# Optimization experiments

Measured on AMD Instinct MI355X. Metric: run time of the kernel, lower is better.

Reference implementation:

```python
import jax, jax.numpy as jnp
import numpy as np


def setup_inputs() -> dict:
    key = jax.random.key(0)
    k1, k2, k3, k4 = jax.random.split(key, 4)
    B, C, T, H, W = 2, 64, 8, 48, 48
    C2 = C // 2
    x_in = jax.random.normal(k1, (B, C, T, H, W), dtype=jnp.float32)
    # per-time-slice 1x1 conv weights (theta/phi pairs), kaiming-ish scale
    theta_w = jax.random.normal(k2, (T, C2, C), dtype=jnp.float32) / np.sqrt(C)
    phi_w = jax.random.normal(k3, (T, C2, C), dtype=jnp.float32) / np.sqrt(C)
    out_w = jax.random.normal(k4, (C, C), dtype=jnp.float32) / np.sqrt(C)
    return {"x_in": x_in, "theta_w": theta_w, "phi_w": phi_w, "out_w": out_w}


def reference(x_in, theta_w, phi_w, out_w):
    B, C, T, H, W = x_in.shape
    C2 = theta_w.shape[1]
    P = H * W
    # [B, T, C, P] layout: flatten spatial, move time next to batch
    x = jnp.transpose(x_in, (0, 2, 1, 3, 4)).reshape(B, T, C, P)
    # per-slice 1x1 convs == per-slice channel matmuls with slice-specific weights
    theta = jnp.einsum("toc,btcp->btop", theta_w, x)  # [B,T,C2,P]
    phi = jnp.einsum("toc,btcp->btop", phi_w, x)      # [B,T,C2,P]
    scale = 1.0 / jnp.sqrt(jnp.asarray(C2, dtype=x_in.dtype))
    scores = jnp.einsum("btcp,btcq->btpq", theta, phi) * scale  # [B,T,P,P]
    attn = jax.nn.softmax(scores, axis=-1)
    f = jnp.einsum("btpq,btcq->btcp", attn, x)  # value = raw x, [B,T,C,P]
    # conv_out: 1x1x1 Conv3d (pointwise over channels), then residual
    out = jnp.einsum("oc,btcp->btop", out_w, f)
    out = jnp.transpose(out.reshape(B, T, C, H, W), (0, 2, 1, 3, 4))
    return out + x_in
```

## Files before the change

### kernel.cpp

```cpp
#include <hip/hip_runtime.h>
#include <hip/hip_bf16.h>

#define CC 64
#define TT 8
#define PP 2304
#define C2 32
#define BT 16
#define NKT 36
#define QKT 9
#define SCALE2 0.25503486f

using h8 = __attribute__((ext_vector_type(8))) _Float16;
using h4 = __attribute__((ext_vector_type(4))) _Float16;
using f4 = __attribute__((ext_vector_type(4))) float;

#if __has_builtin(__builtin_amdgcn_exp2f)
#define EXP2(v) __builtin_amdgcn_exp2f(v)
#else
#define EXP2(v) exp2f(v)
#endif

#define SWIZ_BT(xcd, g) ((xcd) + 8 * ((g) & 1))


__global__ __launch_bounds__(512) void k_prep(
    const float* __restrict__ x, const float* __restrict__ tw,
    const float* __restrict__ pw, _Float16* __restrict__ thf,
    _Float16* __restrict__ rec) {
  const int qt = blockIdx.y >> 1, bt = SWIZ_BT(blockIdx.x, blockIdx.y);
  const int b = bt >> 3, t = bt & 7;
  const int tid = threadIdx.x;
  const int wv = tid >> 6, lane = tid & 63;
  const int quad = lane >> 4, l15 = lane & 15;

  __shared__ __align__(16) float x_s[64][68];
  __shared__ __align__(16) _Float16 th_s[4][16][32];
  __shared__ __align__(16) _Float16 ph_s[4][16][32];

  const size_t xslice = ((size_t)b * CC * TT + t) * PP;
  const int qg0 = qt * 64;
  _Float16* rb = rec + (size_t)(bt * NKT + qt) * 6144;
  const f4 zero = {0.f, 0.f, 0.f, 0.f};

  {
    const int l16 = tid & 15;
    const int crow = tid >> 4;
#pragma unroll
    for (int ppass = 0; ppass < 2; ppass++) {
      const int c = ppass * 32 + crow;
      float4 u = *reinterpret_cast<const float4*>(
          &x[xslice + (size_t)c * (TT * PP) + qg0 + l16 * 4]);
      x_s[l16 * 4 + 0][c] = u.x;
      x_s[l16 * 4 + 1][c] = u.y;
      x_s[l16 * 4 + 2][c] = u.z;
      x_s[l16 * 4 + 3][c] = u.w;
    }
  }
  __syncthreads();

  if (wv < 4) {
    h8 bx[2];
#pragma unroll
    for (int ks = 0; ks < 2; ks++) {
      const float* row = &x_s[wv * 16 + l15][ks * 32 + quad * 8];
      float4 u0 = *reinterpret_cast<const float4*>(row);
      float4 u1 = *reinterpret_cast<const float4*>(row + 4);
      bx[ks][0] = (_Float16)u0.x; bx[ks][1] = (_Float16)u0.y;
      bx[ks][2] = (_Float16)u0.z; bx[ks][3] = (_Float16)u0.w;
      bx[ks][4] = (_Float16)u1.x; bx[ks][5] = (_Float16)u1.y;
      bx[ks][6] = (_Float16)u1.z; bx[ks][7] = (_Float16)u1.w;
    }

    const float* twt = tw + t * C2 * CC;
    const float* pwt = pw + t * C2 * CC;
    f4 accT[2] = {zero, zero}, accP[2] = {zero, zero};
#pragma unroll
    for (int mt = 0; mt < 2; mt++)
#pragma unroll
      for (int ks = 0; ks < 2; ks++) {
        const float* wr = twt + (mt * 16 + l15) * CC + ks * 32 + quad * 8;
        const float* pr = pwt + (mt * 16 + l15) * CC + ks * 32 + quad * 8;
        float4 a0 = *reinterpret_cast<const float4*>(wr);
        float4 a1 = *reinterpret_cast<const float4*>(wr + 4);
        float4 p0 = *reinterpret_cast<const float4*>(pr);
        float4 p1 = *reinterpret_cast<const float4*>(pr + 4);
        h8 at = {(_Float16)a0.x, (_Float16)a0.y, (_Float16)a0.z,
                 (_Float16)a0.w, (_Float16)a1.x, (_Float16)a1.y,
                 (_Float16)a1.z, (_Float16)a1.w};
        h8 ap = {(_Float16)p0.x, (_Float16)p0.y, (_Float16)p0.z,
                 (_Float16)p0.w, (_Float16)p1.x, (_Float16)p1.y,
                 (_Float16)p1.z, (_Float16)p1.w};
        accT[mt] = __builtin_amdgcn_mfma_f32_16x16x32_f16(at, bx[ks],
                                                          accT[mt], 0, 0, 0);
        accP[mt] = __builtin_amdgcn_mfma_f32_16x16x32_f16(ap, bx[ks],
                                                          accP[mt], 0, 0, 0);
      }

#pragma unroll
    for (int mt = 0; mt < 2; mt++) {
      h4 tv, pv;
#pragma unroll
      for (int r = 0; r < 4; r++) {
        tv[r] = (_Float16)(accT[mt][r] * SCALE2);
        pv[r] = (_Float16)accP[mt][r];
      }
      *reinterpret_cast<h4*>(&th_s[wv][l15][mt * 16 + quad * 4]) = tv;
      *reinterpret_cast<h4*>(&ph_s[wv][l15][mt * 16 + quad * 4]) = pv;
    }

    h8 tfrag = *reinterpret_cast<const h8*>(&th_s[wv][l15][quad * 8]);
    *reinterpret_cast<h8*>(
        thf + (((size_t)(bt * NKT + qt) * 4 + wv) * 64 + lane) * 8) = tfrag;

    h8 pfrag = *reinterpret_cast<const h8*>(&ph_s[wv][l15][quad * 8]);
    *reinterpret_cast<h8*>(rb + wv * 512 + lane * 8) = pfrag;
  } else {
    const int w2 = wv - 4;
    const int g = w2 >> 1;
#pragma unroll
    for (int ct2 = 0; ct2 < 2; ct2++) {
      const int ct = (w2 & 1) * 2 + ct2;
      h8 v;
#pragma unroll
      for (int j = 0; j < 4; j++) {
        v[j] = (_Float16)x_s[32 * g + quad * 4 + j][ct * 16 + l15];
        v[4 + j] = (_Float16)x_s[32 * g + 16 + quad * 4 + j][ct * 16 + l15];
      }
      *reinterpret_cast<h8*>(rb + 2048 + (g * 4 + ct) * 512 + lane * 8) = v;
    }
  }
}

__global__ __launch_bounds__(256, 3) void k_attn(
    const float* __restrict__ x, const _Float16* __restrict__ thf,
    const _Float16* __restrict__ rec, const float* __restrict__ ow,
    float* __restrict__ out) {
  const int strip = blockIdx.y >> 1;
  const int bt = SWIZ_BT(blockIdx.x, blockIdx.y);
  const int b = bt >> 3, t = bt & 7;
  const int tid = threadIdx.x;
  const int kg = tid >> 6, lane = tid & 63;
  const int quad = lane >> 4, l15 = lane & 15;

  __shared__ __align__(16) float exch[4 * 3 * 16 * 64];
  __shared__ float exl[4 * 3 * 64];

  h8 bth[3];
#pragma unroll
  for (int pf = 0; pf < 3; pf++)
    bth[pf] = *reinterpret_cast<const h8*>(
        thf + (((size_t)bt * 144 + strip * 3 + pf) * 64 + lane) * 8);

  const _Float16* recb =
      rec + ((size_t)bt * NKT + (size_t)kg * QKT) * 6144 + lane * 8;

  const f4 zero = {0.f, 0.f, 0.f, 0.f};
  f4 O[4][3];
#pragma unroll
  for (int ct = 0; ct < 4; ct++)
#pragma unroll
    for (int pf = 0; pf < 3; pf++) O[ct][pf] = zero;
  float lsum[3] = {0.f, 0.f, 0.f};

  h8 buf[12];

#pragma unroll
  for (int i = 0; i < QKT; i++) {
    const _Float16* _p = recb + (size_t)i * 6144;
#pragma unroll
    for (int j = 0; j < 12; j++)
      buf[j] = *reinterpret_cast<const h8*>(_p + j * 512);

#pragma unroll
    for (int pf = 0; pf < 3; pf++) {
      f4 s[4];
#pragma unroll
      for (int nt = 0; nt < 4; nt++)
        s[nt] = __builtin_amdgcn_mfma_f32_16x16x32_f16(buf[nt], bth[pf], zero,
                                                       0, 0, 0);
#pragma unroll
      for (int g = 0; g < 2; g++) {
        h8 bw;
#pragma unroll
        for (int r = 0; r < 4; r++) {
          float w0 = EXP2(s[2 * g][r]);
          float w1 = EXP2(s[2 * g + 1][r]);
          lsum[pf] += w0 + w1;
          bw[r] = (_Float16)w0;
          bw[4 + r] = (_Float16)w1;
        }
#pragma unroll
        for (int ct = 0; ct < 4; ct++)
          O[ct][pf] = __builtin_amdgcn_mfma_f32_16x16x32_f16(
              buf[4 + g * 4 + ct], bw, O[ct][pf], 0, 0, 0);
      }
    }
  }

#pragma unroll
  for (int pf = 0; pf < 3; pf++) {
    lsum[pf] += __shfl_xor(lsum[pf], 16);
    lsum[pf] += __shfl_xor(lsum[pf], 32);
  }

#pragma unroll
  for (int pf = 0; pf < 3; pf++) {
#pragma unroll
    for (int ct = 0; ct < 4; ct++)
#pragma unroll
      for (int r = 0; r < 4; r++)
        exch[((kg * 3 + pf) * 16 + ct * 4 + r) * 64 + lane] = O[ct][pf][r];
    exl[(kg * 3 + pf) * 64 + lane] = lsum[pf];
  }
  __syncthreads();

  if (kg < 3) {
    float ls = 0.f;
#pragma unroll
    for (int src = 0; src < 4; src++) ls += exl[(src * 3 + kg) * 64 + lane];
    const float inv = 1.f / ls;

    h4 bf[4];
#pragma unroll
    for (int ct = 0; ct < 4; ct++)
#pragma unroll
      for (int r = 0; r < 4; r++) {
        float acc = 0.f;
#pragma unroll
        for (int src = 0; src < 4; src++)
          acc += exch[((src * 3 + kg) * 16 + ct * 4 + r) * 64 + lane];
        bf[ct][r] = (_Float16)(acc * inv);
      }

    f4 D3[4] = {zero, zero, zero, zero};
#pragma unroll
    for (int mt = 0; mt < 4; mt++)
#pragma unroll
      for (int ct = 0; ct < 4; ct++) {
        const float* wrow =
            ow + (size_t)(mt * 16 + l15) * CC + ct * 16 + quad * 4;
        float4 u = *reinterpret_cast<const float4*>(wrow);
        h4 aw = {(_Float16)u.x, (_Float16)u.y, (_Float16)u.z, (_Float16)u.w};
        D3[mt] =
            __builtin_amdgcn_mfma_f32_16x16x16f16(aw, bf[ct], D3[mt], 0, 0, 0);
      }

    const int p0 = strip * 48 + kg * 16 + l15;
#pragma unroll
    for (int mt = 0; mt < 4; mt++)
#pragma unroll
      for (int r = 0; r < 4; r++) {
        const int o = mt * 16 + quad * 4 + r;
        const size_t base = ((size_t)(b * CC + o) * TT + t) * PP + p0;
        out[base] = D3[mt][r] + x[base];
      }
  }
}

extern "C" void kernel_launch(void* const* d_in, const int* in_sizes, int n_in,
                              void* d_out, int out_size, void* d_ws,
                              size_t ws_size, hipStream_t stream) {
  (void)in_sizes; (void)n_in; (void)out_size; (void)ws_size;
  const float* x = (const float*)d_in[0];
  const float* tw = (const float*)d_in[1];
  const float* pw = (const float*)d_in[2];
  const float* ow = (const float*)d_in[3];
  float* out = (float*)d_out;

  _Float16* thf = (_Float16*)d_ws;
  _Float16* rec = thf + (size_t)BT * NKT * 4 * 64 * 8;

  k_prep<<<dim3(8, 72), 512, 0, stream>>>(x, tw, pw, thf, rec);
  k_attn<<<dim3(8, 96), 256, 0, stream>>>(x, thf, rec, ow, out);
}
```

Before: 96.37 us.

## Split attention work by query tile per wave instead of key range

Each of three waves now owns one 16-query tile and iterates over all 36 key tiles, replacing the previous scheme where four waves split the key range and combined partial outputs through shared memory. This removes the LDS exchange, the barrier and the idle fourth wave in the epilogue, and cuts accumulator register use. In exchange, each wave loads every K/V tile independently, which triples global/L2 reads of the rec buffer per block, and each block has fewer waves to hide latency.

```diff
diff --git a/kernel.cpp b/kernel.cpp
--- a/kernel.cpp
+++ b/kernel.cpp
@@ -7,7 +7,6 @@
 #define C2 32
 #define BT 16
 #define NKT 36
-#define QKT 9
 #define SCALE2 0.25503486f
 
 using h8 = __attribute__((ext_vector_type(8))) _Float16;
@@ -131,7 +130,7 @@
   }
 }
 
-__global__ __launch_bounds__(256, 3) void k_attn(
+__global__ __launch_bounds__(192, 3) void k_attn(
     const float* __restrict__ x, const _Float16* __restrict__ thf,
     const _Float16* __restrict__ rec, const float* __restrict__ ow,
     float* __restrict__ out) {
@@ -139,122 +138,81 @@
   const int bt = SWIZ_BT(blockIdx.x, blockIdx.y);
   const int b = bt >> 3, t = bt & 7;
   const int tid = threadIdx.x;
-  const int kg = tid >> 6, lane = tid & 63;
+  const int pf = tid >> 6, lane = tid & 63;
   const int quad = lane >> 4, l15 = lane & 15;
 
-  __shared__ __align__(16) float exch[4 * 3 * 16 * 64];
-  __shared__ float exl[4 * 3 * 64];
-
-  h8 bth[3];
-#pragma unroll
-  for (int pf = 0; pf < 3; pf++)
-    bth[pf] = *reinterpret_cast<const h8*>(
-        thf + (((size_t)bt * 144 + strip * 3 + pf) * 64 + lane) * 8);
-
-  const _Float16* recb =
-      rec + ((size_t)bt * NKT + (size_t)kg * QKT) * 6144 + lane * 8;
+  const h8 bth = *reinterpret_cast<const h8*>(
+      thf + (((size_t)bt * 144 + strip * 3 + pf) * 64 + lane) * 8);
+
+  const _Float16* recb = rec + (size_t)bt * NKT * 6144 + lane * 8;
 
   const f4 zero = {0.f, 0.f, 0.f, 0.f};
-  f4 O[4][3];
-#pragma unroll
-  for (int ct = 0; ct < 4; ct++)
-#pragma unroll
-    for (int pf = 0; pf < 3; pf++) O[ct][pf] = zero;
-  float lsum[3] = {0.f, 0.f, 0.f};
-
-  h8 buf[12];
-
-#pragma unroll
-  for (int i = 0; i < QKT; i++) {
+  f4 O[4];
+#pragma unroll
+  for (int ct = 0; ct < 4; ct++) O[ct] = zero;
+  float lsum = 0.f;
+
+#pragma unroll 2
+  for (int i = 0; i < NKT; i++) {
     const _Float16* _p = recb + (size_t)i * 6144;
+    h8 buf[12];
 #pragma unroll
     for (int j = 0; j < 12; j++)
       buf[j] = *reinterpret_cast<const h8*>(_p + j * 512);
 
-#pragma unroll
-    for (int pf = 0; pf < 3; pf++) {
-      f4 s[4];
-#pragma unroll
-      for (int nt = 0; nt < 4; nt++)
-        s[nt] = __builtin_amdgcn_mfma_f32_16x16x32_f16(buf[nt], bth[pf], zero,
-                                                       0, 0, 0);
-#pragma unroll
-      for (int g = 0; g < 2; g++) {
-        h8 bw;
-#pragma unroll
-        for (int r = 0; r < 4; r++) {
-          float w0 = EXP2(s[2 * g][r]);
-          float w1 = EXP2(s[2 * g + 1][r]);
-          lsum[pf] += w0 + w1;
-          bw[r] = (_Float16)w0;
-          bw[4 + r] = (_Float16)w1;
-        }
-#pragma unroll
-        for (int ct = 0; ct < 4; ct++)
-          O[ct][pf] = __builtin_amdgcn_mfma_f32_16x16x32_f16(
-              buf[4 + g * 4 + ct], bw, O[ct][pf], 0, 0, 0);
-      }
+    f4 s[4];
+#pragma unroll
+    for (int nt = 0; nt < 4; nt++)
+      s[nt] =
+          __builtin_amdgcn_mfma_f32_16x16x32_f16(buf[nt], bth, zero, 0, 0, 0);
+#pragma unroll
+    for (int g = 0; g < 2; g++) {
+      h8 bw;
+#pragma unroll
+      for (int r = 0; r < 4; r++) {
+        float w0 = EXP2(s[2 * g][r]);
+        float w1 = EXP2(s[2 * g + 1][r]);
+        lsum += w0 + w1;
+        bw[r] = (_Float16)w0;
+        bw[4 + r] = (_Float16)w1;
+      }
+#pragma unroll
+      for (int ct = 0; ct < 4; ct++)
+        O[ct] = __builtin_amdgcn_mfma_f32_16x16x32_f16(buf[4 + g * 4 + ct], bw,
+                                                       O[ct], 0, 0, 0);
     }
   }
 
-#pragma unroll
-  for (int pf = 0; pf < 3; pf++) {
-    lsum[pf] += __shfl_xor(lsum[pf], 16);
-    lsum[pf] += __shfl_xor(lsum[pf], 32);
-  }
-
-#pragma unroll
-  for (int pf = 0; pf < 3; pf++) {
-#pragma unroll
-    for (int ct = 0; ct < 4; ct++)
-#pragma unroll
-      for (int r = 0; r < 4; r++)
-        exch[((kg * 3 + pf) * 16 + ct * 4 + r) * 64 + lane] = O[ct][pf][r];
-    exl[(kg * 3 + pf) * 64 + lane] = lsum[pf];
-  }
-  __syncthreads();
-
-  if (kg < 3) {
-    float ls = 0.f;
-#pragma unroll
-    for (int src = 0; src < 4; src++) ls += exl[(src * 3 + kg) * 64 + lane];
-    const float inv = 1.f / ls;
-
-    h4 bf[4];
-#pragma unroll
-    for (int ct = 0; ct < 4; ct++)
-#pragma unroll
-      for (int r = 0; r < 4; r++) {
-        float acc = 0.f;
-#pragma unroll
-        for (int src = 0; src < 4; src++)
-          acc += exch[((src * 3 + kg) * 16 + ct * 4 + r) * 64 + lane];
-        bf[ct][r] = (_Float16)(acc * inv);
-      }
-
-    f4 D3[4] = {zero, zero, zero, zero};
-#pragma unroll
-    for (int mt = 0; mt < 4; mt++)
-#pragma unroll
-      for (int ct = 0; ct < 4; ct++) {
-        const float* wrow =
-            ow + (size_t)(mt * 16 + l15) * CC + ct * 16 + quad * 4;
-        float4 u = *reinterpret_cast<const float4*>(wrow);
-        h4 aw = {(_Float16)u.x, (_Float16)u.y, (_Float16)u.z, (_Float16)u.w};
-        D3[mt] =
-            __builtin_amdgcn_mfma_f32_16x16x16f16(aw, bf[ct], D3[mt], 0, 0, 0);
-      }
-
-    const int p0 = strip * 48 + kg * 16 + l15;
-#pragma unroll
-    for (int mt = 0; mt < 4; mt++)
-#pragma unroll
-      for (int r = 0; r < 4; r++) {
-        const int o = mt * 16 + quad * 4 + r;
-        const size_t base = ((size_t)(b * CC + o) * TT + t) * PP + p0;
-        out[base] = D3[mt][r] + x[base];
-      }
-  }
+  lsum += __shfl_xor(lsum, 16);
+  lsum += __shfl_xor(lsum, 32);
+  const float inv = 1.f / lsum;
+
+  h4 bf[4];
+#pragma unroll
+  for (int ct = 0; ct < 4; ct++)
+#pragma unroll
+    for (int r = 0; r < 4; r++) bf[ct][r] = (_Float16)(O[ct][r] * inv);
+
+  f4 D3[4] = {zero, zero, zero, zero};
+#pragma unroll
+  for (int mt = 0; mt < 4; mt++)
+#pragma unroll
+    for (int ct = 0; ct < 4; ct++) {
+      const float* wrow = ow + (size_t)(mt * 16 + l15) * CC + ct * 16 + quad * 4;
+      float4 u = *reinterpret_cast<const float4*>(wrow);
+      h4 aw = {(_Float16)u.x, (_Float16)u.y, (_Float16)u.z, (_Float16)u.w};
+      D3[mt] = __builtin_amdgcn_mfma_f32_16x16x16f16(aw, bf[ct], D3[mt], 0, 0, 0);
+    }
+
+  const int p0 = strip * 48 + pf * 16 + l15;
+#pragma unroll
+  for (int mt = 0; mt < 4; mt++)
+#pragma unroll
+    for (int r = 0; r < 4; r++) {
+      const int o = mt * 16 + quad * 4 + r;
+      const size_t base = ((size_t)(b * CC + o) * TT + t) * PP + p0;
+      out[base] = D3[mt][r] + x[base];
+    }
 }
 
 extern "C" void kernel_launch(void* const* d_in, const int* in_sizes, int n_in,
@@ -271,5 +229,5 @@
   _Float16* rec = thf + (size_t)BT * NKT * 4 * 64 * 8;
 
   k_prep<<<dim3(8, 72), 512, 0, stream>>>(x, tw, pw, thf, rec);
-  k_attn<<<dim3(8, 96), 256, 0, stream>>>(x, thf, rec, ow, out);
+  k_attn<<<dim3(8, 96), 192, 0, stream>>>(x, thf, rec, ow, out);
 }
```

After: 116.2 us. 20.6% more time.

## Double-buffer half-tile key loads in attention and split prep blocks

Applied to the files above, without the earlier changes.

The attention loop now processes each key tile in two halves and loads the next half into a second register buffer while computing the current one. This is software pipelining meant to hide global load latency behind MFMA and exp work, using fewer registers than the old 12-fragment buffer. The prep kernel is also split into twice as many half-size blocks of 256 threads, each covering 32 positions, to raise parallelism and lower shared memory use per block. There is some risk that the compiler reorders the loads anyway or that register pressure shifts occupancy.

```diff
diff --git a/kernel.cpp b/kernel.cpp
--- a/kernel.cpp
+++ b/kernel.cpp
@@ -23,42 +23,44 @@
 #define SWIZ_BT(xcd, g) ((xcd) + 8 * ((g) & 1))
 
 
-__global__ __launch_bounds__(512) void k_prep(
+__global__ __launch_bounds__(256) void k_prep(
     const float* __restrict__ x, const float* __restrict__ tw,
     const float* __restrict__ pw, _Float16* __restrict__ thf,
     _Float16* __restrict__ rec) {
-  const int qt = blockIdx.y >> 1, bt = SWIZ_BT(blockIdx.x, blockIdx.y);
+  const int bt = SWIZ_BT(blockIdx.x, blockIdx.y);
+  const int qt = blockIdx.y >> 2;
+  const int g = (blockIdx.y >> 1) & 1;
   const int b = bt >> 3, t = bt & 7;
   const int tid = threadIdx.x;
   const int wv = tid >> 6, lane = tid & 63;
   const int quad = lane >> 4, l15 = lane & 15;
 
-  __shared__ __align__(16) float x_s[64][68];
-  __shared__ __align__(16) _Float16 th_s[4][16][32];
-  __shared__ __align__(16) _Float16 ph_s[4][16][32];
+  __shared__ __align__(16) float x_s[32][68];
+  __shared__ __align__(16) _Float16 th_s[2][16][32];
+  __shared__ __align__(16) _Float16 ph_s[2][16][32];
 
   const size_t xslice = ((size_t)b * CC * TT + t) * PP;
-  const int qg0 = qt * 64;
+  const int qg0 = qt * 64 + g * 32;
   _Float16* rb = rec + (size_t)(bt * NKT + qt) * 6144;
   const f4 zero = {0.f, 0.f, 0.f, 0.f};
 
   {
-    const int l16 = tid & 15;
-    const int crow = tid >> 4;
+    const int qoff = (tid & 7) * 4;
+    const int c0 = tid >> 3;
 #pragma unroll
     for (int ppass = 0; ppass < 2; ppass++) {
-      const int c = ppass * 32 + crow;
+      const int c = ppass * 32 + c0;
       float4 u = *reinterpret_cast<const float4*>(
-          &x[xslice + (size_t)c * (TT * PP) + qg0 + l16 * 4]);
-      x_s[l16 * 4 + 0][c] = u.x;
-      x_s[l16 * 4 + 1][c] = u.y;
-      x_s[l16 * 4 + 2][c] = u.z;
-      x_s[l16 * 4 + 3][c] = u.w;
+          &x[xslice + (size_t)c * (TT * PP) + qg0 + qoff]);
+      x_s[qoff + 0][c] = u.x;
+      x_s[qoff + 1][c] = u.y;
+      x_s[qoff + 2][c] = u.z;
+      x_s[qoff + 3][c] = u.w;
     }
   }
   __syncthreads();
 
-  if (wv < 4) {
+  if (wv < 2) {
     h8 bx[2];
 #pragma unroll
     for (int ks = 0; ks < 2; ks++) {
@@ -110,21 +112,21 @@
 
     h8 tfrag = *reinterpret_cast<const h8*>(&th_s[wv][l15][quad * 8]);
     *reinterpret_cast<h8*>(
-        thf + (((size_t)(bt * NKT + qt) * 4 + wv) * 64 + lane) * 8) = tfrag;
+        thf + (((size_t)(bt * 144 + qt * 4 + g * 2 + wv)) * 64 + lane) * 8) =
+        tfrag;
 
     h8 pfrag = *reinterpret_cast<const h8*>(&ph_s[wv][l15][quad * 8]);
-    *reinterpret_cast<h8*>(rb + wv * 512 + lane * 8) = pfrag;
+    *reinterpret_cast<h8*>(rb + (g * 2 + wv) * 512 + lane * 8) = pfrag;
   } else {
-    const int w2 = wv - 4;
-    const int g = w2 >> 1;
+    const int w2 = wv - 2;
 #pragma unroll
     for (int ct2 = 0; ct2 < 2; ct2++) {
-      const int ct = (w2 & 1) * 2 + ct2;
+      const int ct = w2 * 2 + ct2;
       h8 v;
 #pragma unroll
       for (int j = 0; j < 4; j++) {
-        v[j] = (_Float16)x_s[32 * g + quad * 4 + j][ct * 16 + l15];
-        v[4 + j] = (_Float16)x_s[32 * g + 16 + quad * 4 + j][ct * 16 + l15];
+        v[j] = (_Float16)x_s[quad * 4 + j][ct * 16 + l15];
+        v[4 + j] = (_Float16)x_s[16 + quad * 4 + j][ct * 16 + l15];
       }
       *reinterpret_cast<h8*>(rb + 2048 + (g * 4 + ct) * 512 + lane * 8) = v;
     }
@@ -162,40 +164,53 @@
     for (int pf = 0; pf < 3; pf++) O[ct][pf] = zero;
   float lsum[3] = {0.f, 0.f, 0.f};
 
-  h8 buf[12];
-
-#pragma unroll
-  for (int i = 0; i < QKT; i++) {
-    const _Float16* _p = recb + (size_t)i * 6144;
-#pragma unroll
-    for (int j = 0; j < 12; j++)
-      buf[j] = *reinterpret_cast<const h8*>(_p + j * 512);
-
-#pragma unroll
-    for (int pf = 0; pf < 3; pf++) {
-      f4 s[4];
-#pragma unroll
-      for (int nt = 0; nt < 4; nt++)
-        s[nt] = __builtin_amdgcn_mfma_f32_16x16x32_f16(buf[nt], bth[pf], zero,
-                                                       0, 0, 0);
-#pragma unroll
-      for (int g = 0; g < 2; g++) {
-        h8 bw;
-#pragma unroll
-        for (int r = 0; r < 4; r++) {
-          float w0 = EXP2(s[2 * g][r]);
-          float w1 = EXP2(s[2 * g + 1][r]);
-          lsum[pf] += w0 + w1;
-          bw[r] = (_Float16)w0;
-          bw[4 + r] = (_Float16)w1;
-        }
-#pragma unroll
-        for (int ct = 0; ct < 4; ct++)
-          O[ct][pf] = __builtin_amdgcn_mfma_f32_16x16x32_f16(
-              buf[4 + g * 4 + ct], bw, O[ct][pf], 0, 0, 0);
-      }
-    }
-  }
+  h8 hA[6], hB[6];
+
+#define LOADH(BUF, i, gg)                                                    \
+  {                                                                          \
+    const _Float16* _p = recb + (size_t)(i)*6144;                            \
+    BUF[0] = *reinterpret_cast<const h8*>(_p + (2 * (gg)) * 512);            \
+    BUF[1] = *reinterpret_cast<const h8*>(_p + (2 * (gg) + 1) * 512);        \
+    _Pragma("unroll") for (int c = 0; c < 4; c++)                            \
+        BUF[2 + c] =                                                         \
+        *reinterpret_cast<const h8*>(_p + 2048 + ((gg)*4 + c) * 512);        \
+  }
+
+#define COMPH(BUF)                                                          \
+  {                                                                         \
+    _Pragma("unroll") for (int pf = 0; pf < 3; pf++) {                      \
+      f4 sA = __builtin_amdgcn_mfma_f32_16x16x32_f16(BUF[0], bth[pf], zero, \
+                                                     0, 0, 0);              \
+      f4 sB = __builtin_amdgcn_mfma_f32_16x16x32_f16(BUF[1], bth[pf], zero, \
+                                                     0, 0, 0);              \
+      h8 bw;                                                                \
+      _Pragma("unroll") for (int r = 0; r < 4; r++) {                       \
+        float w0 = EXP2(sA[r]);                                             \
+        float w1 = EXP2(sB[r]);                                             \
+        lsum[pf] += w0 + w1;                                                \
+        bw[r] = (_Float16)w0;                                               \
+        bw[4 + r] = (_Float16)w1;                                           \
+      }                                                                     \
+      _Pragma("unroll") for (int ct = 0; ct < 4; ct++)                      \
+          O[ct][pf] = __builtin_amdgcn_mfma_f32_16x16x32_f16(               \
+              BUF[2 + ct], bw, O[ct][pf], 0, 0, 0);                         \
+    }                                                                       \
+  }
+
+  LOADH(hA, 0, 0);
+#pragma unroll
+  for (int h = 0; h < 18; h++) {
+    const int hn = h + 1;
+    if ((h & 1) == 0) {
+      if (hn < 18) LOADH(hB, hn >> 1, hn & 1);
+      COMPH(hA);
+    } else {
+      if (hn < 18) LOADH(hA, hn >> 1, hn & 1);
+      COMPH(hB);
+    }
+  }
+#undef LOADH
+#undef COMPH
 
 #pragma unroll
   for (int pf = 0; pf < 3; pf++) {
@@ -270,6 +285,6 @@
   _Float16* thf = (_Float16*)d_ws;
   _Float16* rec = thf + (size_t)BT * NKT * 4 * 64 * 8;
 
-  k_prep<<<dim3(8, 72), 512, 0, stream>>>(x, tw, pw, thf, rec);
+  k_prep<<<dim3(8, 144), 256, 0, stream>>>(x, tw, pw, thf, rec);
   k_attn<<<dim3(8, 96), 256, 0, stream>>>(x, thf, rec, ow, out);
 }
```

Result: faster. 94.35 us (-2.1%).
